# Optimization experiments

Measured on AMD Instinct MI355X. Metric: run time of the kernel, lower is better.

Reference implementation:

```python
import jax, jax.numpy as jnp
import numpy as np


def _knn_idx(xyz_bn3, k):
    # dist[b,i,j] = ||x_i - x_j||^2 over the point cloud.
    # Faithful to the source: torch.topk defaults to largest=True, so the
    # k+1 LARGEST distances are selected and index 0 (the farthest) is dropped.
    sq = jnp.sum(xyz_bn3 ** 2, axis=-1)  # [b, n]
    dist = sq[:, :, None] + sq[:, None, :] - 2.0 * jnp.einsum('bic,bjc->bij', xyz_bn3, xyz_bn3)
    _, idx = jax.lax.top_k(dist, k + 1)  # largest, sorted descending -> [b, n, k+1]
    return idx[:, :, 1:]  # drop slot 0, keep k neighbors -> [b, n, k]


def setup_inputs() -> dict:
    key = jax.random.key(0)
    B, N, C, K, NB = 8, 4096, 128, 20, 3
    ks = jax.random.split(key, 4)
    scale = 1.0 / np.sqrt(C).astype(np.float32)
    xyz = jax.random.normal(ks[0], (B, 3, N), jnp.float32)
    points = jax.random.normal(ks[1], (B, C, N), jnp.float32)
    W1 = jax.random.normal(ks[2], (NB, C, C), jnp.float32) * scale  # convs[2i] 1x1 kernels
    b1 = jnp.zeros((NB, C), jnp.float32)
    W2 = jax.random.normal(ks[3], (NB, C, C), jnp.float32) * scale  # convs[2i+1] 1x1 kernels
    b2 = jnp.zeros((NB, C), jnp.float32)
    return {"xyz": xyz, "points": points, "W1": W1, "b1": b1, "W2": W2, "b2": b2, "k": K}


def reference(xyz, points, W1, b1, W2, b2, k):
    # xyz: [b, 3, n]; points: [b, C, n]; W1/W2: [n_blocks, C, C]; b1/b2: [n_blocks, C]
    n_blocks = W1.shape[0]
    xyz_bn3 = jnp.transpose(xyz, (0, 2, 1))  # [b, n, 3]
    for i in range(n_blocks):
        shortcut = points
        p = jax.nn.leaky_relu(points, 0.01)  # elementwise, layout [b, C, n]
        # center branch: 1x1 conv == per-point linear
        center = jnp.einsum('oc,bcn->bon', W1[i], p) + b1[i][None, :, None]  # [b, C, n]
        if i == 0:
            idx = _knn_idx(xyz_bn3, k)  # [b, n, k], int32
            # grouping_operation gather: grouped[b,c,n,j] = p[b,c, idx[b,n,j]]
            grouped = jax.vmap(lambda pb, ib: pb[:, ib])(p, idx)  # [b, C, n, k]
            gnn = jnp.einsum('oc,bcnk->bonk', W2[i], grouped) + b2[i][None, :, None, None]
            # mean over concat([center(1 slot), gnn(k slots)], slot axis)
            agg = (center + jnp.sum(gnn, axis=-1)) / (k + 1)
        else:
            # later blocks: grouped_points is just the center point itself (K=1)
            gnn = jnp.einsum('oc,bcn->bon', W2[i], p) + b2[i][None, :, None]
            agg = (center + gnn) * 0.5
        points = agg + shortcut
    return points
```

## Files before the change

### kernel.cpp

```cpp
#include <hip/hip_runtime.h>
#include <math.h>

#define B 8
#define N 4096
#define C 128
#define K 20
#define M (B*N)

__device__ __forceinline__ float lrelu(float x) { return x > 0.f ? x : 0.01f * x; }

typedef float vf16 __attribute__((ext_vector_type(16)));

__global__ void prep_all(const float* __restrict__ xyz,
                         const float* __restrict__ W1, const float* __restrict__ b1,
                         const float* __restrict__ W2, const float* __restrict__ b2,
                         float4* __restrict__ xt, float* __restrict__ wt,
                         float* __restrict__ bias) {
    int blk = blockIdx.x;
    if (blk < 64) {
        int t = blk * 256 + threadIdx.x;
        int c = t >> 7, o = t & 127;
        int oc = o * C + c;
        wt[t]             = W1[oc] * (1.f / 21.f);
        wt[C * C + t]     = W2[oc] * (1.f / 21.f);
        wt[2 * C * C + t] = (W1[C * C + oc] + W2[C * C + oc]) * 0.5f;
        wt[3 * C * C + t] = (W1[2 * C * C + oc] + W2[2 * C * C + oc]) * 0.5f;
        if (t < C) {
            bias[t]         = (b1[t] + 20.f * b2[t]) * (1.f / 21.f);
            bias[C + t]     = (b1[C + t] + b2[C + t]) * 0.5f;
            bias[2 * C + t] = (b1[2 * C + t] + b2[2 * C + t]) * 0.5f;
        }
    } else {
        int t = (blk - 64) * 256 + threadIdx.x;
        int b = t >> 12, n = t & (N - 1);
        const float* p = xyz + (size_t)b * 3 * N;
        float x = p[n], y = p[N + n], z = p[2 * N + n];
        xt[t] = make_float4(x, y, z, x * x + y * y + z * z);
    }
}

__global__ __launch_bounds__(256) void transpose_rs(const float* __restrict__ in,
                                                    float* __restrict__ out, int R, int S) {
    __shared__ float tile[64][65];
    int b = blockIdx.z;
    int r0 = blockIdx.y * 64, s0 = blockIdx.x * 64;
    const float* pin = in + (size_t)b * R * S;
    float* pout = out + (size_t)b * R * S;
    int tr = threadIdx.x >> 4;
    int ts = (threadIdx.x & 15) << 2;
#pragma unroll
    for (int i = 0; i < 4; ++i) {
        int r = tr + i * 16;
        float4 v = *(const float4*)&pin[(size_t)(r0 + r) * S + s0 + ts];
        tile[r][ts + 0] = v.x; tile[r][ts + 1] = v.y;
        tile[r][ts + 2] = v.z; tile[r][ts + 3] = v.w;
    }
    __syncthreads();
#pragma unroll
    for (int i = 0; i < 4; ++i) {
        int s = tr + i * 16;
        float4 v = make_float4(tile[ts + 0][s], tile[ts + 1][s], tile[ts + 2][s], tile[ts + 3][s]);
        *(float4*)&pout[(size_t)(s0 + s) * R + r0 + ts] = v;
    }
}

__global__ __launch_bounds__(256)
__attribute__((amdgpu_waves_per_eu(4, 4)))
void knn_kernel(const float4* __restrict__ xt, int* __restrict__ idx) {
    __shared__ float maxred[4][4];
    __shared__ unsigned int wcnt[2][4][4];
    __shared__ unsigned int cnt[4];
    __shared__ unsigned long long cand[4][128];

    const int tid = threadIdx.x;
    const int wid = tid >> 6, lane = tid & 63;
    const int blk = blockIdx.x;
    const int b = blk >> 10;
    const int i0 = (blk & 1023) << 2;
    const float4* __restrict__ xb = xt + (size_t)b * N;

    float4 xi0 = xb[i0 + 0], xi1 = xb[i0 + 1], xi2 = xb[i0 + 2], xi3 = xb[i0 + 3];
    if (tid < 4) cnt[tid] = 0;

    vf16 d0, d1, d2, d3;
    float mx0 = -1e30f, mx1 = -1e30f, mx2 = -1e30f, mx3 = -1e30f;
#pragma unroll
    for (int u = 0; u < 16; ++u) {
        float4 xj = xb[u * 256 + tid];
        float s0 = fmaf(xi0.x, xj.x, fmaf(xi0.y, xj.y, xi0.z * xj.z));
        float s1 = fmaf(xi1.x, xj.x, fmaf(xi1.y, xj.y, xi1.z * xj.z));
        float s2 = fmaf(xi2.x, xj.x, fmaf(xi2.y, xj.y, xi2.z * xj.z));
        float s3 = fmaf(xi3.x, xj.x, fmaf(xi3.y, xj.y, xi3.z * xj.z));
        float dd0 = xi0.w + xj.w - 2.f * s0;
        float dd1 = xi1.w + xj.w - 2.f * s1;
        float dd2 = xi2.w + xj.w - 2.f * s2;
        float dd3 = xi3.w + xj.w - 2.f * s3;
        d0[u] = dd0; d1[u] = dd1; d2[u] = dd2; d3[u] = dd3;
        mx0 = fmaxf(mx0, dd0); mx1 = fmaxf(mx1, dd1);
        mx2 = fmaxf(mx2, dd2); mx3 = fmaxf(mx3, dd3);
    }
#pragma unroll
    for (int off = 32; off; off >>= 1) {
        mx0 = fmaxf(mx0, __shfl_xor(mx0, off));
        mx1 = fmaxf(mx1, __shfl_xor(mx1, off));
        mx2 = fmaxf(mx2, __shfl_xor(mx2, off));
        mx3 = fmaxf(mx3, __shfl_xor(mx3, off));
    }
    if (lane == 0) {
        maxred[wid][0] = mx0; maxred[wid][1] = mx1;
        maxred[wid][2] = mx2; maxred[wid][3] = mx3;
    }
    __syncthreads();

    float lo[4] = {0.f, 0.f, 0.f, 0.f};
    float hi[4], thr[4];
    bool done[4] = {false, false, false, false};
#pragma unroll
    for (int r = 0; r < 4; ++r) {
        hi[r] = fmaxf(fmaxf(maxred[0][r], maxred[1][r]), fmaxf(maxred[2][r], maxred[3][r]));
        thr[r] = 0.f;
    }

#define COUNT_ROW(dv, r)                                                       \
    if (!done[r]) {                                                            \
        float t_ = 0.5f * (lo[r] + hi[r]);                                     \
        thr[r] = t_;                                                           \
        unsigned int cc_ = 0;                                                  \
        _Pragma("unroll")                                                      \
        for (int u = 0; u < 16; ++u)                                           \
            cc_ += (unsigned int)__popcll(__ballot(dv[u] > t_));               \
        if (lane == 0) wcnt[p][wid][r] = cc_;                                  \
    }

    bool alldone = false;
    for (int it = 0; it < 24 && !alldone; ++it) {
        int p = it & 1;
        COUNT_ROW(d0, 0)
        COUNT_ROW(d1, 1)
        COUNT_ROW(d2, 2)
        COUNT_ROW(d3, 3)
        __syncthreads();
        alldone = true;
#pragma unroll
        for (int r = 0; r < 4; ++r) {
            if (done[r]) continue;
            unsigned int tot = wcnt[p][0][r] + wcnt[p][1][r] + wcnt[p][2][r] + wcnt[p][3][r];
            if (tot >= (unsigned)(K + 1) && tot <= 96u) done[r] = true;
            else if (tot > 96u) lo[r] = thr[r];
            else hi[r] = thr[r];
            if (!done[r]) alldone = false;
        }
    }
#pragma unroll
    for (int r = 0; r < 4; ++r) if (!done[r]) thr[r] = lo[r];

#define COMPACT_ROW(dv, r)                                                     \
    {                                                                          \
        _Pragma("unroll")                                                      \
        for (int u = 0; u < 16; ++u) {                                         \
            bool pred = dv[u] > thr[r];                                        \
            unsigned long long m = __ballot(pred);                             \
            if (m) {                                                           \
                unsigned int base = 0;                                         \
                if (lane == 0) base = atomicAdd(&cnt[r], (unsigned int)__popcll(m)); \
                base = (unsigned int)__shfl((int)base, 0);                     \
                if (pred) {                                                    \
                    unsigned int bel = __builtin_amdgcn_mbcnt_lo((unsigned int)m, 0u); \
                    bel = __builtin_amdgcn_mbcnt_hi((unsigned int)(m >> 32), bel);     \
                    unsigned int pos = base + bel;                             \
                    if (pos < 128u) {                                          \
                        unsigned int j = (unsigned int)(u * 256 + tid);        \
                        cand[r][pos] = ((unsigned long long)__float_as_uint(dv[u]) << 32) \
                                       | (unsigned int)(~j);                   \
                    }                                                          \
                }                                                              \
            }                                                                  \
        }                                                                      \
    }

    COMPACT_ROW(d0, 0)
    COMPACT_ROW(d1, 1)
    COMPACT_ROW(d2, 2)
    COMPACT_ROW(d3, 3)
    __syncthreads();

    {
        int r = wid;
        int row = (b << 12) + i0 + r;
        unsigned int c = cnt[r]; if (c > 128u) c = 128u;
        if (c < (unsigned)(K + 1) && lane < K)
            idx[(size_t)row * K + lane] = (int)lane + 1;
        for (int s = lane; s < (int)c; s += 64) {
            unsigned long long my = cand[r][s];
            int rank = 0;
            for (int q = 0; q < (int)c; ++q) rank += (cand[r][q] > my) ? 1 : 0;
            if (rank >= 1 && rank <= K)
                idx[(size_t)row * K + (rank - 1)] = (int)(~(unsigned int)my);
        }
    }
}

__global__ __launch_bounds__(256) void gather_sum(const float* __restrict__ pt,
                                                  const int* __restrict__ idx,
                                                  float* __restrict__ sT) {
    int t = blockIdx.x * 256 + threadIdx.x;
    int pnt = t >> 5;
    int c4 = (t & 31) << 2;
    int b = pnt >> 12;
    const float* pb = pt + (size_t)b * N * C;
    const int* ip = idx + (size_t)pnt * K;
    float4 acc = make_float4(0.f, 0.f, 0.f, 0.f);
#pragma unroll 4
    for (int k = 0; k < K; ++k) {
        int j = ip[k] & (N - 1);
        float4 v = *(const float4*)&pb[(size_t)j * C + c4];
        acc.x += lrelu(v.x); acc.y += lrelu(v.y);
        acc.z += lrelu(v.z); acc.w += lrelu(v.w);
    }
    *(float4*)&sT[(size_t)pnt * C + c4] = acc;
}

__device__ __forceinline__ void stage_ws(const float* __restrict__ Wt, float (*Ws)[128],
                                         int c0, int tid) {
#pragma unroll
    for (int q = 0; q < 2; ++q) {
        int slot = q * 256 + tid;
        int kk = slot >> 5, oo = (slot & 31) << 2;
        *(float4*)&Ws[kk][oo] = *(const float4*)&Wt[(size_t)(c0 + kk) * C + oo];
    }
}

template<bool LR>
__device__ __forceinline__ void mm_tileP(const float (*P)[132], const float (*Ws)[128],
                                         float acc[4][8], int r0, int o0, int c0) {
#pragma unroll
    for (int q = 0; q < 4; ++q) {
        float4 aj[4];
#pragma unroll
        for (int j = 0; j < 4; ++j) {
            float4 v = *(const float4*)&P[r0 + j][c0 + q * 4];
            if (LR) { v.x = lrelu(v.x); v.y = lrelu(v.y); v.z = lrelu(v.z); v.w = lrelu(v.w); }
            aj[j] = v;
        }
#pragma unroll
        for (int kq = 0; kq < 4; ++kq) {
            int kk = q * 4 + kq;
            float4 w0 = *(const float4*)&Ws[kk][o0];
            float4 w1 = *(const float4*)&Ws[kk][o0 + 64];
#pragma unroll
            for (int j = 0; j < 4; ++j) {
                float a = (kq == 0) ? aj[j].x : (kq == 1) ? aj[j].y : (kq == 2) ? aj[j].z : aj[j].w;
                acc[j][0] = fmaf(a, w0.x, acc[j][0]); acc[j][1] = fmaf(a, w0.y, acc[j][1]);
                acc[j][2] = fmaf(a, w0.z, acc[j][2]); acc[j][3] = fmaf(a, w0.w, acc[j][3]);
                acc[j][4] = fmaf(a, w1.x, acc[j][4]); acc[j][5] = fmaf(a, w1.y, acc[j][5]);
                acc[j][6] = fmaf(a, w1.z, acc[j][6]); acc[j][7] = fmaf(a, w1.w, acc[j][7]);
            }
        }
    }
}

__device__ __forceinline__ void mm_tileA(const float (*As)[20], const float (*Ws)[128],
                                         float acc[4][8], int r0, int o0) {
#pragma unroll
    for (int q = 0; q < 4; ++q) {
        float4 aj[4];
#pragma unroll
        for (int j = 0; j < 4; ++j)
            aj[j] = *(const float4*)&As[r0 + j][q * 4];
#pragma unroll
        for (int kq = 0; kq < 4; ++kq) {
            int kk = q * 4 + kq;
            float4 w0 = *(const float4*)&Ws[kk][o0];
            float4 w1 = *(const float4*)&Ws[kk][o0 + 64];
#pragma unroll
            for (int j = 0; j < 4; ++j) {
                float a = (kq == 0) ? aj[j].x : (kq == 1) ? aj[j].y : (kq == 2) ? aj[j].z : aj[j].w;
                acc[j][0] = fmaf(a, w0.x, acc[j][0]); acc[j][1] = fmaf(a, w0.y, acc[j][1]);
                acc[j][2] = fmaf(a, w0.z, acc[j][2]); acc[j][3] = fmaf(a, w0.w, acc[j][3]);
                acc[j][4] = fmaf(a, w1.x, acc[j][4]); acc[j][5] = fmaf(a, w1.y, acc[j][5]);
                acc[j][6] = fmaf(a, w1.z, acc[j][6]); acc[j][7] = fmaf(a, w1.w, acc[j][7]);
            }
        }
    }
}

__global__ __launch_bounds__(256) void gemm_block0(const float* __restrict__ A0,
                                                   const float* __restrict__ A1,
                                                   const float* __restrict__ Wt0,
                                                   const float* __restrict__ Wt1,
                                                   const float* __restrict__ bias0,
                                                   float* __restrict__ out) {
    __shared__ float P0[64][132];
    __shared__ float As[64][20];
    __shared__ float Ws[16][128];
    const int row0 = blockIdx.x * 64;
    const int tid = threadIdx.x;
    const int r0 = (tid >> 4) << 2;
    const int o0 = (tid & 15) << 2;

#pragma unroll
    for (int q = 0; q < 8; ++q) {
        int s = q * 256 + tid;
        int r = s >> 5, c4 = (s & 31) << 2;
        *(float4*)&P0[r][c4] = *(const float4*)&A0[(size_t)(row0 + r) * C + c4];
    }

    float acc[4][8];
#pragma unroll
    for (int j = 0; j < 4; ++j)
#pragma unroll
        for (int l = 0; l < 8; ++l) acc[j][l] = 0.f;

    for (int c0 = 0; c0 < C; c0 += 16) {
        stage_ws(Wt0, Ws, c0, tid);
        __syncthreads();
        mm_tileP<true>(P0, Ws, acc, r0, o0, c0);
        __syncthreads();
    }
    for (int c0 = 0; c0 < C; c0 += 16) {
        stage_ws(Wt1, Ws, c0, tid);
        {
            int r_ld = tid >> 2, c_ld = (tid & 3) << 2;
            *(float4*)&As[r_ld][c_ld] = *(const float4*)&A1[(size_t)(row0 + r_ld) * C + c0 + c_ld];
        }
        __syncthreads();
        mm_tileA(As, Ws, acc, r0, o0);
        __syncthreads();
    }

    float4 bb0 = *(const float4*)&bias0[o0];
    float4 bb1 = *(const float4*)&bias0[o0 + 64];
#pragma unroll
    for (int j = 0; j < 4; ++j) {
        int rl = r0 + j;
        size_t r = (size_t)(row0 + rl);
        float4 s0 = *(const float4*)&P0[rl][o0];
        float4 s1 = *(const float4*)&P0[rl][o0 + 64];
        float4 v0 = make_float4(acc[j][0] + bb0.x + s0.x, acc[j][1] + bb0.y + s0.y,
                                acc[j][2] + bb0.z + s0.z, acc[j][3] + bb0.w + s0.w);
        float4 v1 = make_float4(acc[j][4] + bb1.x + s1.x, acc[j][5] + bb1.y + s1.y,
                                acc[j][6] + bb1.z + s1.z, acc[j][7] + bb1.w + s1.w);
        *(float4*)&out[r * C + o0] = v0;
        *(float4*)&out[r * C + o0 + 64] = v1;
    }
}

__global__ __launch_bounds__(256) void gemm_block12(const float* __restrict__ A0,
                                                    const float* __restrict__ Wt1,
                                                    const float* __restrict__ Wt2,
                                                    const float* __restrict__ biasAll,
                                                    float* __restrict__ outT) {
    __shared__ float P[64][132];
    __shared__ float Ws[16][128];
    const int row0 = blockIdx.x * 64;
    const int tid = threadIdx.x;
    const int r0 = (tid >> 4) << 2;
    const int o0 = (tid & 15) << 2;

#pragma unroll
    for (int q = 0; q < 8; ++q) {
        int s = q * 256 + tid;
        int r = s >> 5, c4 = (s & 31) << 2;
        *(float4*)&P[r][c4] = *(const float4*)&A0[(size_t)(row0 + r) * C + c4];
    }

    float acc[4][8];
#pragma unroll
    for (int j = 0; j < 4; ++j)
#pragma unroll
        for (int l = 0; l < 8; ++l) acc[j][l] = 0.f;

    for (int c0 = 0; c0 < C; c0 += 16) {
        stage_ws(Wt1, Ws, c0, tid);
        __syncthreads();
        mm_tileP<true>(P, Ws, acc, r0, o0, c0);
        __syncthreads();
    }
    {
        float4 bb0 = *(const float4*)&biasAll[C + o0];
        float4 bb1 = *(const float4*)&biasAll[C + o0 + 64];
#pragma unroll
        for (int j = 0; j < 4; ++j) {
            int rl = r0 + j;
            float4 s0 = *(const float4*)&P[rl][o0];
            float4 s1 = *(const float4*)&P[rl][o0 + 64];
            float4 v0 = make_float4(acc[j][0] + bb0.x + s0.x, acc[j][1] + bb0.y + s0.y,
                                    acc[j][2] + bb0.z + s0.z, acc[j][3] + bb0.w + s0.w);
            float4 v1 = make_float4(acc[j][4] + bb1.x + s1.x, acc[j][5] + bb1.y + s1.y,
                                    acc[j][6] + bb1.z + s1.z, acc[j][7] + bb1.w + s1.w);
            *(float4*)&P[rl][o0] = v0;
            *(float4*)&P[rl][o0 + 64] = v1;
            acc[j][0] = 0.f; acc[j][1] = 0.f; acc[j][2] = 0.f; acc[j][3] = 0.f;
            acc[j][4] = 0.f; acc[j][5] = 0.f; acc[j][6] = 0.f; acc[j][7] = 0.f;
        }
    }
    __syncthreads();
    for (int c0 = 0; c0 < C; c0 += 16) {
        stage_ws(Wt2, Ws, c0, tid);
        __syncthreads();
        mm_tileP<true>(P, Ws, acc, r0, o0, c0);
        __syncthreads();
    }
    {
        float4 bb0 = *(const float4*)&biasAll[2 * C + o0];
        float4 bb1 = *(const float4*)&biasAll[2 * C + o0 + 64];
#pragma unroll
        for (int j = 0; j < 4; ++j) {
            int rl = r0 + j;
            float4 s0 = *(const float4*)&P[rl][o0];
            float4 s1 = *(const float4*)&P[rl][o0 + 64];
            float4 v0 = make_float4(acc[j][0] + bb0.x + s0.x, acc[j][1] + bb0.y + s0.y,
                                    acc[j][2] + bb0.z + s0.z, acc[j][3] + bb0.w + s0.w);
            float4 v1 = make_float4(acc[j][4] + bb1.x + s1.x, acc[j][5] + bb1.y + s1.y,
                                    acc[j][6] + bb1.z + s1.z, acc[j][7] + bb1.w + s1.w);
            *(float4*)&P[rl][o0] = v0;
            *(float4*)&P[rl][o0 + 64] = v1;
        }
    }
    __syncthreads();
    const int o = tid >> 1;
    const int nh = (tid & 1) << 5;
    const int bq = row0 >> 12;
    const int nb = (row0 & (N - 1)) + nh;
    float* po = outT + ((size_t)bq * C + o) * N + nb;
#pragma unroll
    for (int q = 0; q < 8; ++q) {
        int n = nh + q * 4;
        float4 v = make_float4(P[n + 0][o], P[n + 1][o], P[n + 2][o], P[n + 3][o]);
        *(float4*)&po[q * 4] = v;
    }
}

extern "C" void kernel_launch(void* const* d_in, const int* in_sizes, int n_in,
                              void* d_out, int out_size, void* d_ws, size_t ws_size,
                              hipStream_t stream) {
    const float* xyz    = (const float*)d_in[0];
    const float* points = (const float*)d_in[1];
    const float* W1     = (const float*)d_in[2];
    const float* b1     = (const float*)d_in[3];
    const float* W2     = (const float*)d_in[4];
    const float* b2     = (const float*)d_in[5];

    float* ws = (float*)d_ws;
    float4* xt  = (float4*)ws;
    float* pt_a = ws + (size_t)B * N * 4;
    float* pt_b = pt_a + (size_t)M * C;
    float* sT   = pt_b + (size_t)M * C;
    float* wt   = sT + (size_t)M * C;
    float* bias = wt + 4 * C * C;
    int*   idx  = (int*)(bias + 3 * C);

    prep_all<<<192, 256, 0, stream>>>(xyz, W1, b1, W2, b2, xt, wt, bias);
    {
        dim3 g(N / 64, C / 64, B);
        transpose_rs<<<g, 256, 0, stream>>>(points, pt_a, C, N);
    }
    knn_kernel<<<M / 4, 256, 0, stream>>>(xt, idx);
    gather_sum<<<(M * 32) / 256, 256, 0, stream>>>(pt_a, idx, sT);
    gemm_block0<<<M / 64, 256, 0, stream>>>(pt_a, sT, wt, wt + C * C, bias, pt_b);
    gemm_block12<<<M / 64, 256, 0, stream>>>(pt_b, wt + 2 * C * C, wt + 3 * C * C, bias,
                                             (float*)d_out);
}
```

Before: 243.9 us.

## Spread kNN distance rows over 1024-thread blocks with shared atomic counting

The kNN kernel now launches 1024 threads per block, so each thread keeps 4 distances per query row instead of 16. This cuts register pressure and raises the number of active waves. Per-wave count arrays are replaced by LDS atomic accumulators, which need an extra barrier and a reset every bisection iteration. The upper bound for the search is now one max shared by all four rows rather than a per-row max. That looser bound may need more iterations, so the iteration cap rises from 24 to 28.

```diff
diff --git a/kernel.cpp b/kernel.cpp
--- a/kernel.cpp
+++ b/kernel.cpp
@@ -9,7 +9,7 @@
 
 __device__ __forceinline__ float lrelu(float x) { return x > 0.f ? x : 0.01f * x; }
 
-typedef float vf16 __attribute__((ext_vector_type(16)));
+typedef float vf4 __attribute__((ext_vector_type(4)));
 
 __global__ void prep_all(const float* __restrict__ xyz,
                          const float* __restrict__ W1, const float* __restrict__ b1,
@@ -64,12 +64,11 @@
     }
 }
 
-__global__ __launch_bounds__(256)
-__attribute__((amdgpu_waves_per_eu(4, 4)))
+__global__ __launch_bounds__(1024)
 void knn_kernel(const float4* __restrict__ xt, int* __restrict__ idx) {
-    __shared__ float maxred[4][4];
-    __shared__ unsigned int wcnt[2][4][4];
-    __shared__ unsigned int cnt[4];
+    __shared__ float maxred[16];
+    __shared__ unsigned int cnt[2][4];
+    __shared__ unsigned int ccnt[4];
     __shared__ unsigned long long cand[4][128];
 
     const int tid = threadIdx.x;
@@ -80,13 +79,13 @@
     const float4* __restrict__ xb = xt + (size_t)b * N;
 
     float4 xi0 = xb[i0 + 0], xi1 = xb[i0 + 1], xi2 = xb[i0 + 2], xi3 = xb[i0 + 3];
-    if (tid < 4) cnt[tid] = 0;
-
-    vf16 d0, d1, d2, d3;
-    float mx0 = -1e30f, mx1 = -1e30f, mx2 = -1e30f, mx3 = -1e30f;
-#pragma unroll
-    for (int u = 0; u < 16; ++u) {
-        float4 xj = xb[u * 256 + tid];
+    if (tid < 4) { ccnt[tid] = 0; cnt[0][tid] = 0; cnt[1][tid] = 0; }
+
+    vf4 d0, d1, d2, d3;
+    float mxa = -1e30f;
+#pragma unroll
+    for (int u = 0; u < 4; ++u) {
+        float4 xj = xb[u * 1024 + tid];
         float s0 = fmaf(xi0.x, xj.x, fmaf(xi0.y, xj.y, xi0.z * xj.z));
         float s1 = fmaf(xi1.x, xj.x, fmaf(xi1.y, xj.y, xi1.z * xj.z));
         float s2 = fmaf(xi2.x, xj.x, fmaf(xi2.y, xj.y, xi2.z * xj.z));
@@ -96,44 +95,35 @@
         float dd2 = xi2.w + xj.w - 2.f * s2;
         float dd3 = xi3.w + xj.w - 2.f * s3;
         d0[u] = dd0; d1[u] = dd1; d2[u] = dd2; d3[u] = dd3;
-        mx0 = fmaxf(mx0, dd0); mx1 = fmaxf(mx1, dd1);
-        mx2 = fmaxf(mx2, dd2); mx3 = fmaxf(mx3, dd3);
-    }
-#pragma unroll
-    for (int off = 32; off; off >>= 1) {
-        mx0 = fmaxf(mx0, __shfl_xor(mx0, off));
-        mx1 = fmaxf(mx1, __shfl_xor(mx1, off));
-        mx2 = fmaxf(mx2, __shfl_xor(mx2, off));
-        mx3 = fmaxf(mx3, __shfl_xor(mx3, off));
-    }
-    if (lane == 0) {
-        maxred[wid][0] = mx0; maxred[wid][1] = mx1;
-        maxred[wid][2] = mx2; maxred[wid][3] = mx3;
-    }
+        mxa = fmaxf(mxa, fmaxf(fmaxf(dd0, dd1), fmaxf(dd2, dd3)));
+    }
+#pragma unroll
+    for (int off = 32; off; off >>= 1) mxa = fmaxf(mxa, __shfl_xor(mxa, off));
+    if (lane == 0) maxred[wid] = mxa;
     __syncthreads();
+    float hi_all = maxred[0];
+#pragma unroll
+    for (int w = 1; w < 16; ++w) hi_all = fmaxf(hi_all, maxred[w]);
 
     float lo[4] = {0.f, 0.f, 0.f, 0.f};
-    float hi[4], thr[4];
+    float hi[4] = {hi_all, hi_all, hi_all, hi_all};
+    float thr[4] = {0.f, 0.f, 0.f, 0.f};
     bool done[4] = {false, false, false, false};
-#pragma unroll
-    for (int r = 0; r < 4; ++r) {
-        hi[r] = fmaxf(fmaxf(maxred[0][r], maxred[1][r]), fmaxf(maxred[2][r], maxred[3][r]));
-        thr[r] = 0.f;
-    }
 
 #define COUNT_ROW(dv, r)                                                       \
     if (!done[r]) {                                                            \
         float t_ = 0.5f * (lo[r] + hi[r]);                                     \
         thr[r] = t_;                                                           \
         unsigned int cc_ = 0;                                                  \
-        _Pragma("unroll")                                                      \
-        for (int u = 0; u < 16; ++u)                                           \
-            cc_ += (unsigned int)__popcll(__ballot(dv[u] > t_));               \
-        if (lane == 0) wcnt[p][wid][r] = cc_;                                  \
+        cc_ += (unsigned int)__popcll(__ballot(dv[0] > t_));                   \
+        cc_ += (unsigned int)__popcll(__ballot(dv[1] > t_));                   \
+        cc_ += (unsigned int)__popcll(__ballot(dv[2] > t_));                   \
+        cc_ += (unsigned int)__popcll(__ballot(dv[3] > t_));                   \
+        if (lane == 0) atomicAdd(&cnt[p][r], cc_);                             \
     }
 
     bool alldone = false;
-    for (int it = 0; it < 24 && !alldone; ++it) {
+    for (int it = 0; it < 28 && !alldone; ++it) {
         int p = it & 1;
         COUNT_ROW(d0, 0)
         COUNT_ROW(d1, 1)
@@ -144,12 +134,14 @@
 #pragma unroll
         for (int r = 0; r < 4; ++r) {
             if (done[r]) continue;
-            unsigned int tot = wcnt[p][0][r] + wcnt[p][1][r] + wcnt[p][2][r] + wcnt[p][3][r];
+            unsigned int tot = cnt[p][r];
             if (tot >= (unsigned)(K + 1) && tot <= 96u) done[r] = true;
             else if (tot > 96u) lo[r] = thr[r];
             else hi[r] = thr[r];
             if (!done[r]) alldone = false;
         }
+        __syncthreads();
+        if (tid < 4) cnt[p][tid] = 0;
     }
 #pragma unroll
     for (int r = 0; r < 4; ++r) if (!done[r]) thr[r] = lo[r];
@@ -157,19 +149,19 @@
 #define COMPACT_ROW(dv, r)                                                     \
     {                                                                          \
         _Pragma("unroll")                                                      \
-        for (int u = 0; u < 16; ++u) {                                         \
+        for (int u = 0; u < 4; ++u) {                                          \
             bool pred = dv[u] > thr[r];                                        \
             unsigned long long m = __ballot(pred);                             \
             if (m) {                                                           \
                 unsigned int base = 0;                                         \
-                if (lane == 0) base = atomicAdd(&cnt[r], (unsigned int)__popcll(m)); \
+                if (lane == 0) base = atomicAdd(&ccnt[r], (unsigned int)__popcll(m)); \
                 base = (unsigned int)__shfl((int)base, 0);                     \
                 if (pred) {                                                    \
                     unsigned int bel = __builtin_amdgcn_mbcnt_lo((unsigned int)m, 0u); \
                     bel = __builtin_amdgcn_mbcnt_hi((unsigned int)(m >> 32), bel);     \
                     unsigned int pos = base + bel;                             \
                     if (pos < 128u) {                                          \
-                        unsigned int j = (unsigned int)(u * 256 + tid);        \
+                        unsigned int j = (unsigned int)(u * 1024 + tid);       \
                         cand[r][pos] = ((unsigned long long)__float_as_uint(dv[u]) << 32) \
                                        | (unsigned int)(~j);                   \
                     }                                                          \
@@ -184,10 +176,10 @@
     COMPACT_ROW(d3, 3)
     __syncthreads();
 
-    {
+    if (wid < 4) {
         int r = wid;
         int row = (b << 12) + i0 + r;
-        unsigned int c = cnt[r]; if (c > 128u) c = 128u;
+        unsigned int c = ccnt[r]; if (c > 128u) c = 128u;
         if (c < (unsigned)(K + 1) && lane < K)
             idx[(size_t)row * K + lane] = (int)lane + 1;
         for (int s = lane; s < (int)c; s += 64) {
@@ -455,7 +447,7 @@
         dim3 g(N / 64, C / 64, B);
         transpose_rs<<<g, 256, 0, stream>>>(points, pt_a, C, N);
     }
-    knn_kernel<<<M / 4, 256, 0, stream>>>(xt, idx);
+    knn_kernel<<<M / 4, 1024, 0, stream>>>(xt, idx);
     gather_sum<<<(M * 32) / 256, 256, 0, stream>>>(pt_a, idx, sT);
     gemm_block0<<<M / 64, 256, 0, stream>>>(pt_a, sT, wt, wt + C * C, bias, pt_b);
     gemm_block12<<<M / 64, 256, 0, stream>>>(pt_b, wt + 2 * C * C, wt + 3 * C * C, bias,
```

After: 302.2 us. 1.24x slower.
